# Optimization experiments

Hardware: AMD Instinct MI355X
Metric: run time of the kernel (lower is better)

The kernel has to match this reference:

```python
import jax, jax.numpy as jnp
import numpy as np

B, N, H = 8, 512, 256
HEADS, NLAYERS = 8, 3
NEG_SLOPE = 0.2
LN_EPS = 1e-5


def setup_inputs() -> dict:
    key = jax.random.key(0)
    ks = jax.random.split(key, 8)
    emb_inp = jax.random.normal(ks[0], (B, N, H), dtype=jnp.float32)
    rec_inp = jax.random.normal(ks[1], (B, N, 64), dtype=jnp.float32)
    mask = jax.random.randint(ks[2], (B, N, N), 0, 2, dtype=jnp.int32)
    dummy_arg = jnp.zeros((1,), dtype=jnp.float32)
    # GATConv params per layer: lin weight [H, heads*H], att_src/att_dst [heads, H], bias [H]
    W = jax.random.normal(ks[3], (NLAYERS, H, HEADS * H), dtype=jnp.float32) * 0.05
    att_src = jax.random.normal(ks[4], (NLAYERS, HEADS, H), dtype=jnp.float32) * 0.05
    att_dst = jax.random.normal(ks[5], (NLAYERS, HEADS, H), dtype=jnp.float32) * 0.05
    bias = jnp.zeros((NLAYERS, H), dtype=jnp.float32)
    ln_gamma = jnp.ones((H,), dtype=jnp.float32)
    ln_beta = jnp.zeros((H,), dtype=jnp.float32)
    return {"emb_inp": emb_inp, "rec_inp": rec_inp, "mask": mask,
            "dummy_arg": dummy_arg, "W": W, "att_src": att_src,
            "att_dst": att_dst, "bias": bias, "ln_gamma": ln_gamma,
            "ln_beta": ln_beta}


def reference(emb_inp, rec_inp, mask, dummy_arg, W, att_src, att_dst, bias, ln_gamma, ln_beta):
    # mask[b, i, j] != 0 means edge i -> j (PyG: source=row, target=col).
    # adj_t[b, j, i]: does target j receive from source i. GATConv adds self-loops.
    adj_t = jnp.swapaxes(mask, 1, 2).astype(bool) | jnp.eye(N, dtype=bool)[None]
    x = emb_inp
    for l in range(NLAYERS):
        Wl = W[l].reshape(H, HEADS, H)               # per-head projections
        xp = jnp.einsum('bni,ihk->bnhk', x, Wl)      # [B, N, heads, H]
        a_src = jnp.einsum('bnhk,hk->bnh', xp, att_src[l])
        a_dst = jnp.einsum('bnhk,hk->bnh', xp, att_dst[l])
        # logits[b, j(dst), i(src), h] = leaky_relu(a_src_i + a_dst_j)
        logits = jax.nn.leaky_relu(a_dst[:, :, None, :] + a_src[:, None, :, :], NEG_SLOPE)
        logits = jnp.where(adj_t[..., None], logits, -1e9)
        attn = jax.nn.softmax(logits, axis=2)        # softmax over sources per target
        out = jnp.einsum('bjih,bihk->bjhk', attn, xp).mean(axis=2) + bias[l]
        x = x + jax.nn.relu(out)                     # residual + ReLU per GAT layer
    y = emb_inp + jax.nn.relu(x)
    mu = y.mean(-1, keepdims=True)
    var = y.var(-1, keepdims=True)
    return (y - mu) / jnp.sqrt(var + LN_EPS) * ln_gamma + ln_beta
```

## Files before the change

### kernel.cpp

```cpp
#include <hip/hip_runtime.h>

#define BB 8
#define NN 512
#define HH 256
#define NHEADS 8

typedef __attribute__((ext_vector_type(8))) short bf16x8;
typedef __attribute__((ext_vector_type(4))) float f32x4;

__device__ __forceinline__ unsigned f2bf(float f) {
  unsigned u = __float_as_uint(f);
  u += 0x7fffu + ((u >> 16) & 1u);
  return u >> 16;
}
__device__ __forceinline__ float bf2f(unsigned short v) {
  return __uint_as_float(((unsigned)v) << 16);
}

__global__ __launch_bounds__(256) void prologue_kernel(const float* __restrict__ emb,
                                                       const int* __restrict__ mask,
                                                       const float* __restrict__ W,
                                                       float* __restrict__ x,
                                                       unsigned short* __restrict__ x_bf,
                                                       unsigned long long* __restrict__ adjT,
                                                       unsigned short* __restrict__ Wt,
                                                       float* __restrict__ asrcT,
                                                       float* __restrict__ adstT) {
  __shared__ float s[64][65];
  __shared__ unsigned short sadj[4][64];
  const int bid = blockIdx.x;
  const int t = threadIdx.x;
  if (bid < 1024) {
    const int b = bid & 7, chunk = bid >> 3;
    const size_t i4 = ((size_t)b * 128 + chunk) * 256 + t;
    const float4 v = ((const float4*)emb)[i4];
    ((float4*)x)[i4] = v;
    uint2 p;
    p.x = f2bf(v.x) | (f2bf(v.y) << 16);
    p.y = f2bf(v.z) | (f2bf(v.w) << 16);
    ((uint2*)x_bf)[i4] = p;
  } else if (bid < 1536) {
    const int bb = bid - 1024;
    const int b = bb & 7, w = (bb >> 3) & 7, jc = bb >> 6;
    const int jloc = t & 63, qq = t >> 6;
    const int j = jc * 64 + jloc;
    unsigned short bits = 0;
#pragma unroll
    for (int qi = 0; qi < 16; ++qi) {
      const int q = qq * 16 + qi;
      const int i = w * 64 + q;
      const int m = mask[((size_t)b * NN + i) * NN + j];
      if (m != 0 || i == j) bits |= (unsigned short)(1u << qi);
    }
    sadj[qq][jloc] = bits;
    __syncthreads();
    if (t < 64) {
      const unsigned long long word = (unsigned long long)sadj[0][t] |
                                      ((unsigned long long)sadj[1][t] << 16) |
                                      ((unsigned long long)sadj[2][t] << 32) |
                                      ((unsigned long long)sadj[3][t] << 48);
      adjT[((size_t)b * NN + jc * 64 + t) * 8 + w] = word;
    }
  } else if (bid < 1920) {
    const int wb = bid - 1536;
    const int l = wb >> 7;
    const int r = wb & 127;
    const int mt = r & 31, ct = r >> 5;
    const int hk0 = mt * 64, c0 = ct * 64;
    const int tr = t >> 6, tc = t & 63;
#pragma unroll
    for (int p = 0; p < 16; ++p) {
      const int row = p * 4 + tr;
      s[row][tc] = W[(size_t)l * 524288 + (size_t)(c0 + row) * 2048 + hk0 + tc];
    }
    __syncthreads();
#pragma unroll
    for (int p = 0; p < 16; ++p) {
      const int hkl = p * 4 + tr;
      Wt[(size_t)l * 524288 + (size_t)(hk0 + hkl) * 256 + c0 + tc] =
          (unsigned short)f2bf(s[tc][hkl]);
    }
  } else {
    const int i4 = (bid - 1920) * 256 + t;
    const float4 z = {0.f, 0.f, 0.f, 0.f};
    if (i4 < 8192) ((float4*)asrcT)[i4] = z;
    else           ((float4*)adstT)[i4 - 8192] = z;
  }
}

__global__ __launch_bounds__(256, 2) void proj_mfma_kernel(const unsigned short* __restrict__ Wt_l,
                                                           const unsigned short* __restrict__ x_bf,
                                                           const float* __restrict__ att_src_l,
                                                           const float* __restrict__ att_dst_l,
                                                           unsigned short* __restrict__ xpTT,
                                                           float* __restrict__ asrcT,
                                                           float* __restrict__ adstT) {
  __shared__ __align__(16) unsigned char lds[32768];
  const int t = threadIdx.x;
  const int lane = t & 63, wave = t >> 6;
  const int wj = wave >> 1, wk = wave & 1;

  const int bid = blockIdx.x;
  const int b = bid & 7;
  const int r = bid >> 3;
  const int mt = r & 15, nt = r >> 4;
  const int hk0 = mt * 128, n0 = nt * 128;

  const int tr = t >> 1, th = t & 1;
  const size_t aBase = (size_t)(hk0 + tr) * 256 + th * 16;
  const size_t bBase = ((size_t)(b * NN + n0 + tr)) * 256 + th * 16;
  const unsigned sw_w = ((tr >> 1) & 3) << 4;
  const unsigned w0 = tr * 64 + ((th * 32 + 0) ^ sw_w);
  const unsigned w1 = tr * 64 + ((th * 32 + 16) ^ sw_w);

  uint4 ra0, ra1, rb0, rb1;
  {
    ra0 = *(const uint4*)(Wt_l + aBase);
    ra1 = *(const uint4*)(Wt_l + aBase + 8);
    rb0 = *(const uint4*)(x_bf + bBase);
    rb1 = *(const uint4*)(x_bf + bBase + 8);
  }

  const f32x4 z4 = {0.f, 0.f, 0.f, 0.f};
  f32x4 acc[4][4];
#pragma unroll
  for (int fr = 0; fr < 4; ++fr)
#pragma unroll
    for (int fc = 0; fc < 4; ++fc) acc[fr][fc] = z4;

  for (int s = 0; s < 8; ++s) {
    const unsigned boff = (s & 1) << 14;
    *(uint4*)(lds + boff + w0) = ra0;
    *(uint4*)(lds + boff + w1) = ra1;
    *(uint4*)(lds + boff + 8192 + w0) = rb0;
    *(uint4*)(lds + boff + 8192 + w1) = rb1;
    __syncthreads();
    if (s < 7) {
      const size_t off = (size_t)(s + 1) * 32;
      ra0 = *(const uint4*)(Wt_l + aBase + off);
      ra1 = *(const uint4*)(Wt_l + aBase + off + 8);
      rb0 = *(const uint4*)(x_bf + bBase + off);
      rb1 = *(const uint4*)(x_bf + bBase + off + 8);
    }
    bf16x8 af[4], bfr[4];
#pragma unroll
    for (int fr = 0; fr < 4; ++fr) {
      const int rA = wj * 64 + fr * 16 + (lane & 15);
      af[fr] = *(const bf16x8*)(lds + boff + rA * 64 +
                                (((lane >> 4) * 16) ^ (((rA >> 1) & 3) << 4)));
    }
#pragma unroll
    for (int fc = 0; fc < 4; ++fc) {
      const int rB = wk * 64 + fc * 16 + (lane & 15);
      bfr[fc] = *(const bf16x8*)(lds + boff + 8192 + rB * 64 +
                                 (((lane >> 4) * 16) ^ (((rB >> 1) & 3) << 4)));
    }
#pragma unroll
    for (int fr = 0; fr < 4; ++fr)
#pragma unroll
      for (int fc = 0; fc < 4; ++fc)
        acc[fr][fc] = __builtin_amdgcn_mfma_f32_16x16x32_bf16(af[fr], bfr[fc], acc[fr][fc], 0, 0, 0);
  }

  __syncthreads();
  unsigned short* sc = (unsigned short*)lds;
  const int lr = lane & 15, lo = lane >> 4;
#pragma unroll
  for (int fr = 0; fr < 4; ++fr) {
    const int rowl0 = wj * 64 + fr * 16 + lo * 4;
#pragma unroll
    for (int fc = 0; fc < 4; ++fc) {
      const int coll = wk * 64 + fc * 16 + lr;
#pragma unroll
      for (int rr = 0; rr < 4; ++rr)
        sc[(rowl0 + rr) * 128 + coll] = (unsigned short)f2bf(acc[fr][fc][rr]);
    }
  }
  __syncthreads();
  unsigned short* xpb = xpTT + (size_t)b * 2048 * NN;
#pragma unroll
  for (int p = 0; p < 8; ++p) {
    const int idx4 = p * 256 + t;
    const int row = idx4 >> 4;
    const int c4 = idx4 & 15;
    *(uint4*)(xpb + (size_t)(hk0 + row) * NN + n0 + c4 * 8) = *(const uint4*)(sc + idx4 * 8);
  }

  float wsv[4][4], wdv[4][4];
#pragma unroll
  for (int fr = 0; fr < 4; ++fr) {
    const int row0 = hk0 + wj * 64 + fr * 16 + lo * 4;
#pragma unroll
    for (int rr = 0; rr < 4; ++rr) {
      wsv[fr][rr] = att_src_l[row0 + rr];
      wdv[fr][rr] = att_dst_l[row0 + rr];
    }
  }
  const int bh = b * 8 + (mt >> 1);
#pragma unroll
  for (int fc = 0; fc < 4; ++fc) {
    float as = 0.f, ad = 0.f;
#pragma unroll
    for (int fr = 0; fr < 4; ++fr)
#pragma unroll
      for (int rr = 0; rr < 4; ++rr) {
        as = fmaf(acc[fr][fc][rr], wsv[fr][rr], as);
        ad = fmaf(acc[fr][fc][rr], wdv[fr][rr], ad);
      }
    as += __shfl_xor(as, 16);
    as += __shfl_xor(as, 32);
    ad += __shfl_xor(ad, 16);
    ad += __shfl_xor(ad, 32);
    if ((lane >> 4) == 0) {
      const int col = n0 + wk * 64 + fc * 16 + lane;
      atomicAdd(&asrcT[(size_t)bh * NN + col], as);
      atomicAdd(&adstT[(size_t)bh * NN + col], ad);
    }
  }
}

__global__ __launch_bounds__(256, 2) void agg_fused_kernel(const unsigned short* __restrict__ xpTT,
                                                           const float* __restrict__ asrcT,
                                                           const float* __restrict__ adstT,
                                                           const unsigned long long* __restrict__ adjT,
                                                           float* __restrict__ out_part) {
  __shared__ __align__(16) unsigned char lds[40960];
  __shared__ float s_as[NN];
  __shared__ __align__(16) unsigned char s_adjw[4096];
  __shared__ float s_dinv[64];
  const int t = threadIdx.x;
  const int lane = t & 63, wave = t >> 6;
  const int wk = wave;

  const int bid = blockIdx.x;
  const int b = bid & 7;
  const int r = bid >> 3;
  const int jt = r & 7, hs = r >> 3;
  const int j0 = jt * 64;
  const int bh = b * 8 + hs;

  const int tr4 = t >> 2, th4 = t & 3;
  const int tr2 = t >> 1, th2 = t & 1;

  s_as[t] = asrcT[(size_t)bh * NN + t];
  s_as[t + 256] = asrcT[(size_t)bh * NN + t + 256];
  *(uint4*)(s_adjw + tr4 * 64 + th4 * 16) =
      *(const uint4*)((const unsigned char*)adjT + ((size_t)(b * NN + j0 + tr4)) * 64 + th4 * 16);
  const float adv = adstT[(size_t)bh * NN + j0 + tr4];
  __syncthreads();

  const unsigned sw4 = ((tr4 >> 1) & 3) << 4;
  const unsigned wA = tr4 * 64 + ((th4 * 16) ^ sw4);
  const unsigned sw2 = ((tr2 >> 1) & 3) << 4;
  const unsigned wB0 = tr2 * 64 + ((th2 * 32 + 0) ^ sw2);
  const unsigned wB1 = tr2 * 64 + ((th2 * 32 + 16) ^ sw2);
  const size_t bBase0 = ((size_t)bh * HH + tr2) * NN + th2 * 16;
  const size_t bBase1 = ((size_t)bh * HH + tr2 + 128) * NN + th2 * 16;

  float esum = 0.f;
  uint4 pe, rb0, rb1, rb2, rb3;
  auto GENP = [&](int s, uint4& o) {
    const unsigned bits = s_adjw[tr4 * 64 + s * 4 + th4];
    const float* ap = s_as + s * 32 + th4 * 8;
    unsigned wds[4];
#pragma unroll
    for (int p = 0; p < 4; ++p) {
      float z0 = adv + ap[2 * p];
      float z1 = adv + ap[2 * p + 1];
      z0 = fmaxf(z0, 0.2f * z0);
      z1 = fmaxf(z1, 0.2f * z1);
      float e0 = __expf(z0);
      float e1 = __expf(z1);
      e0 = ((bits >> (2 * p)) & 1u) ? e0 : 0.f;
      e1 = ((bits >> (2 * p + 1)) & 1u) ? e1 : 0.f;
      esum += e0 + e1;
      wds[p] = f2bf(e0) | (f2bf(e1) << 16);
    }
    o.x = wds[0]; o.y = wds[1]; o.z = wds[2]; o.w = wds[3];
  };
  auto BLOAD = [&](int s, uint4& r0, uint4& r1, uint4& r2, uint4& r3) {
    r0 = *(const uint4*)(xpTT + bBase0 + s * 32);
    r1 = *(const uint4*)(xpTT + bBase0 + s * 32 + 8);
    r2 = *(const uint4*)(xpTT + bBase1 + s * 32);
    r3 = *(const uint4*)(xpTT + bBase1 + s * 32 + 8);
  };

  GENP(0, pe);
  BLOAD(0, rb0, rb1, rb2, rb3);

  const f32x4 z4 = {0.f, 0.f, 0.f, 0.f};
  f32x4 acc[4][4];
#pragma unroll
  for (int fr = 0; fr < 4; ++fr)
#pragma unroll
    for (int fc = 0; fc < 4; ++fc) acc[fr][fc] = z4;

  for (int s = 0; s < 16; ++s) {
    const unsigned boff = (s & 1) ? 20480u : 0u;
    *(uint4*)(lds + boff + wA) = pe;
    *(uint4*)(lds + boff + 4096 + wB0) = rb0;
    *(uint4*)(lds + boff + 4096 + wB1) = rb1;
    *(uint4*)(lds + boff + 4096 + wB0 + 8192) = rb2;
    *(uint4*)(lds + boff + 4096 + wB1 + 8192) = rb3;
    __syncthreads();
    if (s < 15) {
      BLOAD(s + 1, rb0, rb1, rb2, rb3);
      GENP(s + 1, pe);
    }
    bf16x8 af[4], bfr[4];
#pragma unroll
    for (int fr = 0; fr < 4; ++fr) {
      const int rA = fr * 16 + (lane & 15);
      af[fr] = *(const bf16x8*)(lds + boff + rA * 64 +
                                (((lane >> 4) * 16) ^ (((rA >> 1) & 3) << 4)));
    }
#pragma unroll
    for (int fc = 0; fc < 4; ++fc) {
      const int rB = wk * 64 + fc * 16 + (lane & 15);
      bfr[fc] = *(const bf16x8*)(lds + boff + 4096 + rB * 64 +
                                 (((lane >> 4) * 16) ^ (((rB >> 1) & 3) << 4)));
    }
#pragma unroll
    for (int fr = 0; fr < 4; ++fr)
#pragma unroll
      for (int fc = 0; fc < 4; ++fc)
        acc[fr][fc] = __builtin_amdgcn_mfma_f32_16x16x32_bf16(af[fr], bfr[fc], acc[fr][fc], 0, 0, 0);
  }

  esum += __shfl_xor(esum, 1);
  esum += __shfl_xor(esum, 2);
  __syncthreads();
  if (th4 == 0) s_dinv[tr4] = 1.f / (8.f * esum);
  __syncthreads();

  float* op = out_part + ((size_t)hs * BB + b) * NN * HH;
#pragma unroll
  for (int fr = 0; fr < 4; ++fr) {
    const int jl0 = fr * 16 + (lane >> 4) * 4;
#pragma unroll
    for (int fc = 0; fc < 4; ++fc) {
      const int kcol = wk * 64 + fc * 16 + (lane & 15);
#pragma unroll
      for (int rr = 0; rr < 4; ++rr)
        op[(size_t)(j0 + jl0 + rr) * HH + kcol] = acc[fr][fc][rr] * s_dinv[jl0 + rr];
    }
  }
}

__global__ __launch_bounds__(256) void out_epi_kernel(const float* __restrict__ out_part,
                                                      const float* __restrict__ bias_l,
                                                      float* __restrict__ x,
                                                      unsigned short* __restrict__ x_bf,
                                                      float* __restrict__ asrcT,
                                                      float* __restrict__ adstT) {
  const int bid = blockIdx.x;
  const int t = threadIdx.x;
  if (bid < 64) {
    const int i4 = bid * 256 + t;
    const float4 z = {0.f, 0.f, 0.f, 0.f};
    if (i4 < 8192) ((float4*)asrcT)[i4] = z;
    else           ((float4*)adstT)[i4 - 8192] = z;
  }
  const int b = bid & 7, nn = bid >> 3;
  const size_t idx = ((size_t)(b * NN + nn)) * HH + t;
  const size_t S = (size_t)BB * NN * HH;
  float o = bias_l[t];
#pragma unroll
  for (int s = 0; s < 8; ++s) o += out_part[s * S + idx];
  const float xn = x[idx] + fmaxf(o, 0.f);
  x[idx] = xn;
  x_bf[idx] = (unsigned short)f2bf(xn);
}

__global__ __launch_bounds__(256) void epi_ln_kernel(const float* __restrict__ out_part,
                                                     const float* __restrict__ bias_l,
                                                     const float* __restrict__ x,
                                                     const float* __restrict__ emb,
                                                     const float* __restrict__ gamma,
                                                     const float* __restrict__ beta,
                                                     float* __restrict__ out) {
  const int bid = blockIdx.x;
  const int t = threadIdx.x;
  const int b = bid & 7, nn = bid >> 3;
  const size_t idx = ((size_t)(b * NN + nn)) * HH + t;
  const size_t S = (size_t)BB * NN * HH;
  float o = bias_l[t];
#pragma unroll
  for (int s = 0; s < 8; ++s) o += out_part[s * S + idx];
  const float xn = x[idx] + fmaxf(o, 0.f);
  const float y = emb[idx] + fmaxf(xn, 0.f);
  float s1 = y, s2 = y * y;
#pragma unroll
  for (int off = 32; off > 0; off >>= 1) {
    s1 += __shfl_down(s1, off);
    s2 += __shfl_down(s2, off);
  }
  __shared__ float rs[4], rs2[4], stat[2];
  const int wave = t >> 6, lane = t & 63;
  if (lane == 0) { rs[wave] = s1; rs2[wave] = s2; }
  __syncthreads();
  if (t == 0) {
    const float S1 = rs[0] + rs[1] + rs[2] + rs[3];
    const float S2 = rs2[0] + rs2[1] + rs2[2] + rs2[3];
    const float mu = S1 * (1.f / 256.f);
    const float var = S2 * (1.f / 256.f) - mu * mu;
    stat[0] = mu;
    stat[1] = rsqrtf(var + 1e-5f);
  }
  __syncthreads();
  out[idx] = (y - stat[0]) * stat[1] * gamma[t] + beta[t];
}

extern "C" void kernel_launch(void* const* d_in, const int* in_sizes, int n_in,
                              void* d_out, int out_size, void* d_ws, size_t ws_size,
                              hipStream_t stream) {
  const float* emb    = (const float*)d_in[0];
  const int*   mask   = (const int*)d_in[2];
  const float* W      = (const float*)d_in[4];
  const float* aw_src = (const float*)d_in[5];
  const float* aw_dst = (const float*)d_in[6];
  const float* bias   = (const float*)d_in[7];
  const float* gamma  = (const float*)d_in[8];
  const float* beta   = (const float*)d_in[9];
  float* out = (float*)d_out;

  char* ws = (char*)d_ws;
  unsigned short* xpTT = (unsigned short*)(ws);
  float* out_part      = (float*)(ws + 16777216);
  float* x             = (float*)(ws + 50331648);
  unsigned short* x_bf = (unsigned short*)(ws + 54525952);
  float* asrcT         = (float*)(ws + 56623104);
  float* adstT         = (float*)(ws + 56754176);
  unsigned long long* adjT = (unsigned long long*)(ws + 57016320);
  unsigned short* Wt   = (unsigned short*)(ws + 57278464);

  prologue_kernel<<<1984, 256, 0, stream>>>(emb, mask, W, x, x_bf, adjT, Wt, asrcT, adstT);

  for (int l = 0; l < 3; ++l) {
    proj_mfma_kernel<<<512, 256, 0, stream>>>(Wt + (size_t)l * 524288, x_bf,
                                              aw_src + l * NHEADS * HH, aw_dst + l * NHEADS * HH,
                                              xpTT, asrcT, adstT);
    agg_fused_kernel<<<512, 256, 0, stream>>>(xpTT, asrcT, adstT, adjT, out_part);
    if (l < 2)
      out_epi_kernel<<<BB * NN, 256, 0, stream>>>(out_part, bias + l * HH, x, x_bf, asrcT, adstT);
  }
  epi_ln_kernel<<<BB * NN, 256, 0, stream>>>(out_part, bias + 2 * HH, x, emb, gamma, beta, out);
}
```

Baseline: 127.6 us.

## Fuse epilogue and layernorm into aggregation via last-block atomic counter

Removes the separate out_epi and epi_ln kernel launches. The last of the 8 head-blocks for each (batch, row-tile) now reduces the partial outputs and applies the residual, or in the final layer the layernorm, selected by an atomic counter. Per-layer asrc/adst buffers are zeroed once in the prologue instead of being cleared inside the epilogue kernel. The reduction now runs on only 64 blocks with a serial loop over 64 rows, so it has less parallelism and extra fences, in exchange for fewer launches.

```diff
diff --git a/kernel.cpp b/kernel.cpp
--- a/kernel.cpp
+++ b/kernel.cpp
@@ -25,7 +25,8 @@
                                                        unsigned long long* __restrict__ adjT,
                                                        unsigned short* __restrict__ Wt,
                                                        float* __restrict__ asrcT,
-                                                       float* __restrict__ adstT) {
+                                                       float* __restrict__ adstT,
+                                                       unsigned* __restrict__ cnt) {
   __shared__ float s[64][65];
   __shared__ unsigned short sadj[4][64];
   const int bid = blockIdx.x;
@@ -83,8 +84,9 @@
   } else {
     const int i4 = (bid - 1920) * 256 + t;
     const float4 z = {0.f, 0.f, 0.f, 0.f};
-    if (i4 < 8192) ((float4*)asrcT)[i4] = z;
-    else           ((float4*)adstT)[i4 - 8192] = z;
+    if (i4 < 24576) ((float4*)asrcT)[i4] = z;
+    else            ((float4*)adstT)[i4 - 24576] = z;
+    if (bid == 1920 && t < 192) cnt[t] = 0u;
   }
 }
 
@@ -93,8 +95,8 @@
                                                            const float* __restrict__ att_src_l,
                                                            const float* __restrict__ att_dst_l,
                                                            unsigned short* __restrict__ xpTT,
-                                                           float* __restrict__ asrcT,
-                                                           float* __restrict__ adstT) {
+                                                           float* __restrict__ asrcT_l,
+                                                           float* __restrict__ adstT_l) {
   __shared__ __align__(16) unsigned char lds[32768];
   const int t = threadIdx.x;
   const int lane = t & 63, wave = t >> 6;
@@ -213,21 +215,32 @@
     ad += __shfl_xor(ad, 32);
     if ((lane >> 4) == 0) {
       const int col = n0 + wk * 64 + fc * 16 + lane;
-      atomicAdd(&asrcT[(size_t)bh * NN + col], as);
-      atomicAdd(&adstT[(size_t)bh * NN + col], ad);
+      atomicAdd(&asrcT_l[(size_t)bh * NN + col], as);
+      atomicAdd(&adstT_l[(size_t)bh * NN + col], ad);
     }
   }
 }
 
 __global__ __launch_bounds__(256, 2) void agg_fused_kernel(const unsigned short* __restrict__ xpTT,
-                                                           const float* __restrict__ asrcT,
-                                                           const float* __restrict__ adstT,
+                                                           const float* __restrict__ asrcT_l,
+                                                           const float* __restrict__ adstT_l,
                                                            const unsigned long long* __restrict__ adjT,
-                                                           float* __restrict__ out_part) {
+                                                           float* __restrict__ out_part,
+                                                           const float* __restrict__ bias_l,
+                                                           float* __restrict__ x,
+                                                           unsigned short* __restrict__ x_bf,
+                                                           const float* __restrict__ emb,
+                                                           const float* __restrict__ gamma,
+                                                           const float* __restrict__ beta,
+                                                           float* __restrict__ out,
+                                                           unsigned* __restrict__ cnt_l,
+                                                           const int mode) {
   __shared__ __align__(16) unsigned char lds[40960];
   __shared__ float s_as[NN];
   __shared__ __align__(16) unsigned char s_adjw[4096];
   __shared__ float s_dinv[64];
+  __shared__ float s_mu[64], s_rsig[64];
+  __shared__ int s_last;
   const int t = threadIdx.x;
   const int lane = t & 63, wave = t >> 6;
   const int wk = wave;
@@ -242,11 +255,11 @@
   const int tr4 = t >> 2, th4 = t & 3;
   const int tr2 = t >> 1, th2 = t & 1;
 
-  s_as[t] = asrcT[(size_t)bh * NN + t];
-  s_as[t + 256] = asrcT[(size_t)bh * NN + t + 256];
+  s_as[t] = asrcT_l[(size_t)bh * NN + t];
+  s_as[t + 256] = asrcT_l[(size_t)bh * NN + t + 256];
   *(uint4*)(s_adjw + tr4 * 64 + th4 * 16) =
       *(const uint4*)((const unsigned char*)adjT + ((size_t)(b * NN + j0 + tr4)) * 64 + th4 * 16);
-  const float adv = adstT[(size_t)bh * NN + j0 + tr4];
+  const float adv = adstT_l[(size_t)bh * NN + j0 + tr4];
   __syncthreads();
 
   const unsigned sw4 = ((tr4 >> 1) & 3) << 4;
@@ -345,70 +358,70 @@
         op[(size_t)(j0 + jl0 + rr) * HH + kcol] = acc[fr][fc][rr] * s_dinv[jl0 + rr];
     }
   }
-}
-
-__global__ __launch_bounds__(256) void out_epi_kernel(const float* __restrict__ out_part,
-                                                      const float* __restrict__ bias_l,
-                                                      float* __restrict__ x,
-                                                      unsigned short* __restrict__ x_bf,
-                                                      float* __restrict__ asrcT,
-                                                      float* __restrict__ adstT) {
-  const int bid = blockIdx.x;
-  const int t = threadIdx.x;
-  if (bid < 64) {
-    const int i4 = bid * 256 + t;
-    const float4 z = {0.f, 0.f, 0.f, 0.f};
-    if (i4 < 8192) ((float4*)asrcT)[i4] = z;
-    else           ((float4*)adstT)[i4 - 8192] = z;
-  }
-  const int b = bid & 7, nn = bid >> 3;
-  const size_t idx = ((size_t)(b * NN + nn)) * HH + t;
+
+  __threadfence();
+  __syncthreads();
+  if (t == 0) {
+    const unsigned old = __hip_atomic_fetch_add(&cnt_l[b * 8 + jt], 1u,
+                                                __ATOMIC_ACQ_REL, __HIP_MEMORY_SCOPE_AGENT);
+    s_last = (old == 7u) ? 1 : 0;
+  }
+  __syncthreads();
+  if (!s_last) return;
+  __threadfence();
+
   const size_t S = (size_t)BB * NN * HH;
-  float o = bias_l[t];
-#pragma unroll
-  for (int s = 0; s < 8; ++s) o += out_part[s * S + idx];
-  const float xn = x[idx] + fmaxf(o, 0.f);
-  x[idx] = xn;
-  x_bf[idx] = (unsigned short)f2bf(xn);
-}
-
-__global__ __launch_bounds__(256) void epi_ln_kernel(const float* __restrict__ out_part,
-                                                     const float* __restrict__ bias_l,
-                                                     const float* __restrict__ x,
-                                                     const float* __restrict__ emb,
-                                                     const float* __restrict__ gamma,
-                                                     const float* __restrict__ beta,
-                                                     float* __restrict__ out) {
-  const int bid = blockIdx.x;
-  const int t = threadIdx.x;
-  const int b = bid & 7, nn = bid >> 3;
-  const size_t idx = ((size_t)(b * NN + nn)) * HH + t;
-  const size_t S = (size_t)BB * NN * HH;
-  float o = bias_l[t];
-#pragma unroll
-  for (int s = 0; s < 8; ++s) o += out_part[s * S + idx];
-  const float xn = x[idx] + fmaxf(o, 0.f);
-  const float y = emb[idx] + fmaxf(xn, 0.f);
-  float s1 = y, s2 = y * y;
-#pragma unroll
-  for (int off = 32; off > 0; off >>= 1) {
-    s1 += __shfl_down(s1, off);
-    s2 += __shfl_down(s2, off);
-  }
-  __shared__ float rs[4], rs2[4], stat[2];
-  const int wave = t >> 6, lane = t & 63;
-  if (lane == 0) { rs[wave] = s1; rs2[wave] = s2; }
-  __syncthreads();
-  if (t == 0) {
-    const float S1 = rs[0] + rs[1] + rs[2] + rs[3];
-    const float S2 = rs2[0] + rs2[1] + rs2[2] + rs2[3];
-    const float mu = S1 * (1.f / 256.f);
-    const float var = S2 * (1.f / 256.f) - mu * mu;
-    stat[0] = mu;
-    stat[1] = rsqrtf(var + 1e-5f);
-  }
-  __syncthreads();
-  out[idx] = (y - stat[0]) * stat[1] * gamma[t] + beta[t];
+  if (mode < 2) {
+#pragma unroll 4
+    for (int rr = 0; rr < 64; ++rr) {
+      const size_t idx = ((size_t)(b * NN + j0 + rr)) * HH + t;
+      float o = bias_l[t];
+#pragma unroll
+      for (int s = 0; s < 8; ++s) o += out_part[s * S + idx];
+      const float xn = x[idx] + fmaxf(o, 0.f);
+      x[idx] = xn;
+      x_bf[idx] = (unsigned short)f2bf(xn);
+    }
+  } else {
+#pragma unroll 4
+    for (int rr = 0; rr < 64; ++rr) {
+      const size_t idx = ((size_t)(b * NN + j0 + rr)) * HH + t;
+      float o = bias_l[t];
+#pragma unroll
+      for (int s = 0; s < 8; ++s) o += out_part[s * S + idx];
+      const float xn = x[idx] + fmaxf(o, 0.f);
+      out[idx] = emb[idx] + fmaxf(xn, 0.f);
+    }
+    __syncthreads();
+    {
+      const int jr = t >> 2, q = t & 3;
+      const size_t rb = ((size_t)(b * NN + j0 + jr)) * HH + q * 64;
+      float s1 = 0.f, s2 = 0.f;
+#pragma unroll 8
+      for (int c = 0; c < 64; ++c) {
+        const float y = out[rb + c];
+        s1 += y;
+        s2 += y * y;
+      }
+      s1 += __shfl_xor(s1, 1);
+      s1 += __shfl_xor(s1, 2);
+      s2 += __shfl_xor(s2, 1);
+      s2 += __shfl_xor(s2, 2);
+      if (q == 0) {
+        const float mu = s1 * (1.f / 256.f);
+        const float var = s2 * (1.f / 256.f) - mu * mu;
+        s_mu[jr] = mu;
+        s_rsig[jr] = rsqrtf(var + 1e-5f);
+      }
+    }
+    __syncthreads();
+    const float g = gamma[t], be = beta[t];
+#pragma unroll 4
+    for (int rr = 0; rr < 64; ++rr) {
+      const size_t idx = ((size_t)(b * NN + j0 + rr)) * HH + t;
+      out[idx] = (out[idx] - s_mu[rr]) * s_rsig[rr] * g + be;
+    }
+  }
 }
 
 extern "C" void kernel_launch(void* const* d_in, const int* in_sizes, int n_in,
@@ -430,19 +443,21 @@
   float* x             = (float*)(ws + 50331648);
   unsigned short* x_bf = (unsigned short*)(ws + 54525952);
   float* asrcT         = (float*)(ws + 56623104);
-  float* adstT         = (float*)(ws + 56754176);
-  unsigned long long* adjT = (unsigned long long*)(ws + 57016320);
-  unsigned short* Wt   = (unsigned short*)(ws + 57278464);
-
-  prologue_kernel<<<1984, 256, 0, stream>>>(emb, mask, W, x, x_bf, adjT, Wt, asrcT, adstT);
+  float* adstT         = (float*)(ws + 57016320);
+  unsigned long long* adjT = (unsigned long long*)(ws + 57409536);
+  unsigned short* Wt   = (unsigned short*)(ws + 57671680);
+  unsigned* cnt        = (unsigned*)(ws + 60817408);
+
+  prologue_kernel<<<2112, 256, 0, stream>>>(emb, mask, W, x, x_bf, adjT, Wt, asrcT, adstT, cnt);
 
   for (int l = 0; l < 3; ++l) {
+    float* asrc_l = asrcT + (size_t)l * 32768;
+    float* adst_l = adstT + (size_t)l * 32768;
     proj_mfma_kernel<<<512, 256, 0, stream>>>(Wt + (size_t)l * 524288, x_bf,
                                               aw_src + l * NHEADS * HH, aw_dst + l * NHEADS * HH,
-                                              xpTT, asrcT, adstT);
-    agg_fused_kernel<<<512, 256, 0, stream>>>(xpTT, asrcT, adstT, adjT, out_part);
-    if (l < 2)
-      out_epi_kernel<<<BB * NN, 256, 0, stream>>>(out_part, bias + l * HH, x, x_bf, asrcT, adstT);
-  }
-  epi_ln_kernel<<<BB * NN, 256, 0, stream>>>(out_part, bias + 2 * HH, x, emb, gamma, beta, out);
-}
+                                              xpTT, asrc_l, adst_l);
+    agg_fused_kernel<<<512, 256, 0, stream>>>(xpTT, asrc_l, adst_l, adjT, out_part,
+                                              bias + l * HH, x, x_bf, emb, gamma, beta, out,
+                                              cnt + l * 64, l);
+  }
+}
```

Result: slower. 367.3 us (+187.8%).
